# Performance work log

Hardware: AMD Instinct MI355X
Metric: run time of the kernel (lower is better)

## Reference

```python
import jax, jax.numpy as jnp
import numpy as np

B, T, H = 16, 64, 256  # batch, timesteps (= num stacked layers), hidden
L = T                  # MultiRNNCell([cell]*timesteps): layers == timesteps, shared weights


def setup_inputs() -> dict:
    key = jax.random.key(0)
    k1, k2, k3 = jax.random.split(key, 3)
    x = jax.random.normal(k1, (B, T, H), dtype=jnp.float32)
    init_state = jax.random.normal(k2, (L, 2, B, H), dtype=jnp.float32) * 0.1  # [L, (c,h), B, H]
    W = jax.random.normal(k3, (2 * H, 4 * H), dtype=jnp.float32) / np.sqrt(2 * H)
    b = jnp.zeros((4 * H,), dtype=jnp.float32)
    return {"x": x, "init_state": init_state, "W": W, "b": b}


def reference(x, init_state, W, b):
    # TF LSTMCell math: gates order (i, j, f, o), forget_bias = 1.0
    c0 = init_state[:, 0]  # [L,B,H]
    h0 = init_state[:, 1]  # [L,B,H]

    def layer_fn(inp, st):
        # inp: [B,H] input to this layer; st = (c,h) each [B,H]
        lc, lh = st
        z = jnp.concatenate([inp, lh], axis=-1) @ W + b  # [B,4H]
        i, j, f, o = jnp.split(z, 4, axis=-1)
        nc = jax.nn.sigmoid(f + 1.0) * lc + jax.nn.sigmoid(i) * jnp.tanh(j)
        nh = jax.nn.sigmoid(o) * jnp.tanh(nc)
        return nh, (nc, nh)  # carry = input to next layer; ys = new per-layer state

    def step(carry, xt):
        # carry: (c,h) each [L,B,H]; xt: [B,H]
        c, h = carry
        top_h, (nc, nh) = jax.lax.scan(layer_fn, xt, (c, h))
        return (nc, nh), top_h

    (_, _), ys = jax.lax.scan(step, (c0, h0), jnp.transpose(x, (1, 0, 2)))  # ys: [T,B,H]
    return jnp.transpose(ys, (1, 0, 2))  # [B,T,H] top-layer outputs (dynamic_rnn outputs)
```

## Files before the change

### kernel.cpp

```cpp
#include <hip/hip_runtime.h>

typedef _Float16 half8 __attribute__((ext_vector_type(8)));
typedef float f32x4 __attribute__((ext_vector_type(4)));

#define SCOPE __HIP_MEMORY_SCOPE_AGENT

constexpr size_t OFF_FLAGS = 0;
constexpr size_t OFF_H     = 65536;

__device__ __forceinline__ size_t Hidx(int slot, int l, int b, int u) {
  return (((size_t)slot * 64 + l) * 16 + b) * 256 + u;
}
__device__ __forceinline__ float sigm(float v) { return 1.0f / (1.0f + __expf(-v)); }
__device__ __forceinline__ float tanh_(float v) { return 1.0f - 2.0f / (__expf(2.0f * v) + 1.0f); }

__global__ void init_ws(const float* __restrict__ init_state, char* ws) {
  int* flags = (int*)(ws + OFF_FLAGS);
  _Float16* Hp = (_Float16*)(ws + OFF_H);
  const int tid = blockIdx.x * 256 + threadIdx.x;
  if (tid < 4096) flags[tid] = 0;
  for (int e = tid; e < 64 * 16 * 256; e += 65536) {
    const int u = e & 255, b = (e >> 8) & 15, l = e >> 12;
    Hp[Hidx(1, l, b, u)] = (_Float16)init_state[((l * 2 + 1) * 16 + b) * 256 + u];
  }
}

__device__ __forceinline__ void spin_ge4(int* p) {
  for (int it = 0; it < 4000000; ++it) {
    if (__hip_atomic_load(p, __ATOMIC_RELAXED, SCOPE) >= 4) return;
    __builtin_amdgcn_s_sleep(1);
  }
}

__global__ __launch_bounds__(256, 1) void lstm_mfma(
    const float* __restrict__ x, const float* __restrict__ init_state,
    const float* __restrict__ W, const float* __restrict__ bias,
    float* __restrict__ out, char* ws) {
  int* flags = (int*)(ws + OFF_FLAGS);
  unsigned long long* Hp64 = (unsigned long long*)(ws + OFF_H);

  const int tid = threadIdx.x;
  const int wg = blockIdx.x;
  const int l = wg >> 2, r = wg & 3;
  const int wv = tid >> 6, lane = tid & 63;

  __shared__ alignas(16) _Float16 aLds[16 * 64 * 8];
  __shared__ alignas(16) float zLds[16 * 260];
  __shared__ unsigned short hLds[16 * 64];

  half8 wreg[64];
#pragma unroll
  for (int q = 0; q < 4; ++q) {
    const int nl = (wv * 4 + q) * 16 + (lane & 15);
    const int col = (nl & 3) * 256 + r * 64 + (nl >> 2);
#pragma unroll
    for (int kb = 0; kb < 16; ++kb) {
      const int k0 = kb * 32 + (lane >> 4) * 8;
      const float* src = W + (size_t)k0 * 1024 + col;
      half8 hv;
#pragma unroll
      for (int jj = 0; jj < 8; ++jj) hv[jj] = (_Float16)src[(size_t)jj * 1024];
      wreg[q * 16 + kb] = hv;
    }
  }

  const int hu = tid & 63, b4 = tid >> 6;
  const int gu = r * 64 + hu;
  float creg[4];
#pragma unroll
  for (int bi = 0; bi < 4; ++bi)
    creg[bi] = init_state[((l * 2 + 0) * 16 + (b4 * 4 + bi)) * 256 + gu];
  const float bi_ = bias[0 * 256 + gu], bj_ = bias[1 * 256 + gu];
  const float bf_ = bias[2 * 256 + gu], bo_ = bias[3 * 256 + gu];

  for (int t = 0; t < 64; ++t) {
    const int slotCur = t & 1, slotPrev = (t + 1) & 1;

    if (tid == 0) {
      if (l > 0) spin_ge4(&flags[(l - 1) * 64 + t]);
      if (t > 0) spin_ge4(&flags[l * 64 + (t - 1)]);
      if (t >= 2 && l < 63) spin_ge4(&flags[(l + 1) * 64 + (t - 2)]);
    }
    __syncthreads();

#pragma unroll
    for (int i = 0; i < 4; ++i) {
      const int e = i * 256 + tid;
      const int kb = e >> 6, ln = e & 63;
      const int m = ln & 15, k0 = kb * 32 + (ln >> 4) * 8;
      _Float16* dst = &aLds[(size_t)(kb * 64 + ln) * 8];
      if (kb < 8) {
        if (l == 0) {
          const float* xs = x + ((size_t)m * 64 + t) * 256 + k0;
          half8 hv;
#pragma unroll
          for (int jj = 0; jj < 8; ++jj) hv[jj] = (_Float16)xs[jj];
          *(half8*)dst = hv;
        } else {
          const size_t b64 = Hidx(slotCur, l - 1, m, k0) >> 2;
          unsigned long long a0 = __hip_atomic_load(Hp64 + b64, __ATOMIC_RELAXED, SCOPE);
          unsigned long long a1 = __hip_atomic_load(Hp64 + b64 + 1, __ATOMIC_RELAXED, SCOPE);
          ((unsigned long long*)dst)[0] = a0;
          ((unsigned long long*)dst)[1] = a1;
        }
      } else {
        const size_t b64 = Hidx(slotPrev, l, m, k0 - 256) >> 2;
        unsigned long long a0 = __hip_atomic_load(Hp64 + b64, __ATOMIC_RELAXED, SCOPE);
        unsigned long long a1 = __hip_atomic_load(Hp64 + b64 + 1, __ATOMIC_RELAXED, SCOPE);
        ((unsigned long long*)dst)[0] = a0;
        ((unsigned long long*)dst)[1] = a1;
      }
    }
    __syncthreads();

    f32x4 acc[4] = {{0.f, 0.f, 0.f, 0.f}, {0.f, 0.f, 0.f, 0.f},
                    {0.f, 0.f, 0.f, 0.f}, {0.f, 0.f, 0.f, 0.f}};
#pragma unroll
    for (int kb = 0; kb < 16; ++kb) {
      half8 a = *(const half8*)&aLds[(kb * 64 + lane) * 8];
#pragma unroll
      for (int q = 0; q < 4; ++q)
        acc[q] = __builtin_amdgcn_mfma_f32_16x16x32_f16(a, wreg[q * 16 + kb], acc[q], 0, 0, 0);
    }

#pragma unroll
    for (int q = 0; q < 4; ++q) {
      const int nl = (wv * 4 + q) * 16 + (lane & 15);
      const int m0 = (lane >> 4) * 4;
#pragma unroll
      for (int rg = 0; rg < 4; ++rg) zLds[(m0 + rg) * 260 + nl] = acc[q][rg];
    }
    __syncthreads();

#pragma unroll
    for (int bi = 0; bi < 4; ++bi) {
      const int b = b4 * 4 + bi;
      f32x4 zg = *(const f32x4*)&zLds[b * 260 + hu * 4];
      const float iv = zg[0] + bi_, jv = zg[1] + bj_;
      const float fv = zg[2] + bf_, ov = zg[3] + bo_;
      const float nc = sigm(fv + 1.0f) * creg[bi] + sigm(iv) * tanh_(jv);
      const float nh = sigm(ov) * tanh_(nc);
      creg[bi] = nc;
      union { _Float16 f; unsigned short s; } cv;
      cv.f = (_Float16)nh;
      hLds[b * 64 + hu] = cv.s;
      if (l == 63) out[((size_t)b * 64 + t) * 256 + gu] = nh;
    }
    __syncthreads();

    {
      const int b = tid >> 4, u0 = (tid & 15) * 4;
      unsigned long long v = *(unsigned long long*)&hLds[b * 64 + u0];
      __hip_atomic_store(Hp64 + (Hidx(slotCur, l, b, r * 64 + u0) >> 2), v,
                         __ATOMIC_RELAXED, SCOPE);
    }
    __syncthreads();
    if (tid == 0)
      __hip_atomic_fetch_add(&flags[l * 64 + t], 1, __ATOMIC_RELEASE, SCOPE);
  }
}

extern "C" void kernel_launch(void* const* d_in, const int* in_sizes, int n_in,
                              void* d_out, int out_size, void* d_ws,
                              size_t ws_size, hipStream_t stream) {
  const float* x          = (const float*)d_in[0];
  const float* init_state = (const float*)d_in[1];
  const float* W          = (const float*)d_in[2];
  const float* bias       = (const float*)d_in[3];
  float* out = (float*)d_out;
  char* ws   = (char*)d_ws;

  init_ws<<<256, 256, 0, stream>>>(init_state, ws);
  lstm_mfma<<<256, 256, 0, stream>>>(x, init_state, W, bias, out, ws);
}
```

Measured before the change: 784.7 us.

## Replace flag counters with timestep-tagged data words for LSTM wavefront sync

Replaces the per-(layer,timestep) counter flags, spun on by a single thread, with 64-bit words that pack two fp16 hidden values and a 16-bit timestep tag. Each thread polls its own input words until the tags match, so data and readiness arrive in one load. The intent is to drop the release/acquire handoff and the extra barrier and store round-trip on the critical path between layers. It adds a per-workgroup progress counter for backpressure and a slow-path check. It doubles the bytes per hidden value and relies on the 64-bit relaxed atomic stores being seen whole by readers.

```diff
diff --git a/kernel.cpp b/kernel.cpp
--- a/kernel.cpp
+++ b/kernel.cpp
@@ -5,30 +5,29 @@
 
 #define SCOPE __HIP_MEMORY_SCOPE_AGENT
 
-constexpr size_t OFF_FLAGS = 0;
-constexpr size_t OFF_H     = 65536;
-
-__device__ __forceinline__ size_t Hidx(int slot, int l, int b, int u) {
-  return (((size_t)slot * 64 + l) * 16 + b) * 256 + u;
+constexpr size_t OFF_PROG = 0;
+constexpr size_t OFF_H    = 65536;
+constexpr size_t SLOT_STRIDE = (size_t)64 * 16 * 128;
+
+__device__ __forceinline__ size_t Widx(int l, int b, int wi) {
+  return ((size_t)l * 16 + b) * 128 + wi;
 }
 __device__ __forceinline__ float sigm(float v) { return 1.0f / (1.0f + __expf(-v)); }
 __device__ __forceinline__ float tanh_(float v) { return 1.0f - 2.0f / (__expf(2.0f * v) + 1.0f); }
 
 __global__ void init_ws(const float* __restrict__ init_state, char* ws) {
-  int* flags = (int*)(ws + OFF_FLAGS);
-  _Float16* Hp = (_Float16*)(ws + OFF_H);
+  int* prog = (int*)(ws + OFF_PROG);
+  unsigned long long* Hw = (unsigned long long*)(ws + OFF_H);
   const int tid = blockIdx.x * 256 + threadIdx.x;
-  if (tid < 4096) flags[tid] = 0;
-  for (int e = tid; e < 64 * 16 * 256; e += 65536) {
-    const int u = e & 255, b = (e >> 8) & 15, l = e >> 12;
-    Hp[Hidx(1, l, b, u)] = (_Float16)init_state[((l * 2 + 1) * 16 + b) * 256 + u];
-  }
-}
-
-__device__ __forceinline__ void spin_ge4(int* p) {
-  for (int it = 0; it < 4000000; ++it) {
-    if (__hip_atomic_load(p, __ATOMIC_RELAXED, SCOPE) >= 4) return;
-    __builtin_amdgcn_s_sleep(1);
+  if (tid < 256) prog[tid] = -1;
+  for (int e = tid; e < 64 * 16 * 128; e += 65536) {
+    const int wi = e & 127, b = (e >> 7) & 15, l = e >> 11;
+    Hw[Widx(l, b, wi)] = 0xFFFE00000000ULL;
+    union { _Float16 f; unsigned short s; } h0, h1;
+    h0.f = (_Float16)init_state[((l * 2 + 1) * 16 + b) * 256 + 2 * wi];
+    h1.f = (_Float16)init_state[((l * 2 + 1) * 16 + b) * 256 + 2 * wi + 1];
+    Hw[SLOT_STRIDE + Widx(l, b, wi)] =
+        (unsigned long long)h0.s | ((unsigned long long)h1.s << 16) | (0xFFFFULL << 32);
   }
 }
 
@@ -36,8 +35,8 @@
     const float* __restrict__ x, const float* __restrict__ init_state,
     const float* __restrict__ W, const float* __restrict__ bias,
     float* __restrict__ out, char* ws) {
-  int* flags = (int*)(ws + OFF_FLAGS);
-  unsigned long long* Hp64 = (unsigned long long*)(ws + OFF_H);
+  int* prog = (int*)(ws + OFF_PROG);
+  unsigned long long* Hw = (unsigned long long*)(ws + OFF_H);
 
   const int tid = threadIdx.x;
   const int wg = blockIdx.x;
@@ -68,50 +67,96 @@
   const int gu = r * 64 + hu;
   float creg[4];
 #pragma unroll
-  for (int bi = 0; bi < 4; ++bi)
-    creg[bi] = init_state[((l * 2 + 0) * 16 + (b4 * 4 + bi)) * 256 + gu];
+  for (int bb = 0; bb < 4; ++bb)
+    creg[bb] = init_state[((l * 2 + 0) * 16 + (b4 * 4 + bb)) * 256 + gu];
   const float bi_ = bias[0 * 256 + gu], bj_ = bias[1 * 256 + gu];
   const float bf_ = bias[2 * 256 + gu], bo_ = bias[3 * 256 + gu];
 
+  int kbA[4], lnA[4];
+  size_t wbase[4];
+#pragma unroll
+  for (int i = 0; i < 4; ++i) {
+    const int e = i * 256 + tid, kb = e >> 6, ln = e & 63;
+    const int m = ln & 15, k0 = kb * 32 + (ln >> 4) * 8;
+    kbA[i] = kb; lnA[i] = ln;
+    wbase[i] = (i < 2) ? (l > 0 ? Widx(l - 1, m, k0 >> 1) : 0)
+                       : Widx(l, m, (k0 - 256) >> 1);
+  }
+
   for (int t = 0; t < 64; ++t) {
     const int slotCur = t & 1, slotPrev = (t + 1) & 1;
-
-    if (tid == 0) {
-      if (l > 0) spin_ge4(&flags[(l - 1) * 64 + t]);
-      if (t > 0) spin_ge4(&flags[l * 64 + (t - 1)]);
-      if (t >= 2 && l < 63) spin_ge4(&flags[(l + 1) * 64 + (t - 2)]);
+    const unsigned short tagIn = (unsigned short)t;
+    const unsigned short tagOwn = (unsigned short)(t - 1);
+
+    if (l == 0) {
+#pragma unroll
+      for (int i = 0; i < 2; ++i) {
+        const int kb = kbA[i], ln = lnA[i];
+        const int m = ln & 15, k0 = kb * 32 + (ln >> 4) * 8;
+        const float* xs = x + ((size_t)m * 64 + t) * 256 + k0;
+        half8 hv;
+#pragma unroll
+        for (int jj = 0; jj < 8; ++jj) hv[jj] = (_Float16)xs[jj];
+        *(half8*)&aLds[(size_t)(kb * 64 + ln) * 8] = hv;
+      }
+    }
+
+    unsigned pend = (l == 0) ? 0xFF00u : 0xFFFFu;
+    bool bp = !(tid == 0 && l < 63 && t >= 2);
+    int round = 0;
+    while (pend || !bp) {
+      bool fast = true;
+      if (round >= 2 && l > 0 && (pend & 0x00FFu)) {
+        int pl = __hip_atomic_load(&prog[(l - 1) * 4 + r], __ATOMIC_RELAXED, SCOPE);
+        fast = (pl >= t);
+      }
+      if (fast && pend) {
+        unsigned long long wv_[16];
+#pragma unroll
+        for (int i = 0; i < 4; ++i) {
+          const unsigned long long* sp =
+              Hw + ((i < 2 ? slotCur : slotPrev) ? SLOT_STRIDE : 0) + wbase[i];
+#pragma unroll
+          for (int j = 0; j < 4; ++j) {
+            const int b_ = i * 4 + j;
+            if ((pend >> b_) & 1u)
+              wv_[b_] = __hip_atomic_load(sp + j, __ATOMIC_RELAXED, SCOPE);
+          }
+        }
+#pragma unroll
+        for (int i = 0; i < 4; ++i) {
+          unsigned* dp = (unsigned*)&aLds[(size_t)(kbA[i] * 64 + lnA[i]) * 8];
+          const unsigned short exp_ = (i < 2) ? tagIn : tagOwn;
+#pragma unroll
+          for (int j = 0; j < 4; ++j) {
+            const int b_ = i * 4 + j;
+            if ((pend >> b_) & 1u) {
+              const unsigned long long wd = wv_[b_];
+              if ((unsigned short)(wd >> 32) == exp_) {
+                dp[j] = (unsigned)wd;
+                pend &= ~(1u << b_);
+              }
+            }
+          }
+        }
+      }
+      if (!bp) {
+        const int need = t - 2;
+        int p0 = __hip_atomic_load(&prog[(l + 1) * 4 + 0], __ATOMIC_RELAXED, SCOPE);
+        int p1 = __hip_atomic_load(&prog[(l + 1) * 4 + 1], __ATOMIC_RELAXED, SCOPE);
+        int p2 = __hip_atomic_load(&prog[(l + 1) * 4 + 2], __ATOMIC_RELAXED, SCOPE);
+        int p3 = __hip_atomic_load(&prog[(l + 1) * 4 + 3], __ATOMIC_RELAXED, SCOPE);
+        bp = (p0 >= need) && (p1 >= need) && (p2 >= need) && (p3 >= need);
+      }
+      if (pend || !bp) {
+        ++round;
+        if (round > 4000000) break;
+        if (fast) __builtin_amdgcn_s_sleep(1);
+        else      __builtin_amdgcn_s_sleep(16);
+      }
     }
     __syncthreads();
-
-#pragma unroll
-    for (int i = 0; i < 4; ++i) {
-      const int e = i * 256 + tid;
-      const int kb = e >> 6, ln = e & 63;
-      const int m = ln & 15, k0 = kb * 32 + (ln >> 4) * 8;
-      _Float16* dst = &aLds[(size_t)(kb * 64 + ln) * 8];
-      if (kb < 8) {
-        if (l == 0) {
-          const float* xs = x + ((size_t)m * 64 + t) * 256 + k0;
-          half8 hv;
-#pragma unroll
-          for (int jj = 0; jj < 8; ++jj) hv[jj] = (_Float16)xs[jj];
-          *(half8*)dst = hv;
-        } else {
-          const size_t b64 = Hidx(slotCur, l - 1, m, k0) >> 2;
-          unsigned long long a0 = __hip_atomic_load(Hp64 + b64, __ATOMIC_RELAXED, SCOPE);
-          unsigned long long a1 = __hip_atomic_load(Hp64 + b64 + 1, __ATOMIC_RELAXED, SCOPE);
-          ((unsigned long long*)dst)[0] = a0;
-          ((unsigned long long*)dst)[1] = a1;
-        }
-      } else {
-        const size_t b64 = Hidx(slotPrev, l, m, k0 - 256) >> 2;
-        unsigned long long a0 = __hip_atomic_load(Hp64 + b64, __ATOMIC_RELAXED, SCOPE);
-        unsigned long long a1 = __hip_atomic_load(Hp64 + b64 + 1, __ATOMIC_RELAXED, SCOPE);
-        ((unsigned long long*)dst)[0] = a0;
-        ((unsigned long long*)dst)[1] = a1;
-      }
-    }
-    __syncthreads();
+    if (tid == 0) __hip_atomic_store(&prog[wg], t, __ATOMIC_RELAXED, SCOPE);
 
     f32x4 acc[4] = {{0.f, 0.f, 0.f, 0.f}, {0.f, 0.f, 0.f, 0.f},
                     {0.f, 0.f, 0.f, 0.f}, {0.f, 0.f, 0.f, 0.f}};
@@ -133,14 +178,14 @@
     __syncthreads();
 
 #pragma unroll
-    for (int bi = 0; bi < 4; ++bi) {
-      const int b = b4 * 4 + bi;
+    for (int bb = 0; bb < 4; ++bb) {
+      const int b = b4 * 4 + bb;
       f32x4 zg = *(const f32x4*)&zLds[b * 260 + hu * 4];
       const float iv = zg[0] + bi_, jv = zg[1] + bj_;
       const float fv = zg[2] + bf_, ov = zg[3] + bo_;
-      const float nc = sigm(fv + 1.0f) * creg[bi] + sigm(iv) * tanh_(jv);
+      const float nc = sigm(fv + 1.0f) * creg[bb] + sigm(iv) * tanh_(jv);
       const float nh = sigm(ov) * tanh_(nc);
-      creg[bi] = nc;
+      creg[bb] = nc;
       union { _Float16 f; unsigned short s; } cv;
       cv.f = (_Float16)nh;
       hLds[b * 64 + hu] = cv.s;
@@ -149,14 +194,17 @@
     __syncthreads();
 
     {
-      const int b = tid >> 4, u0 = (tid & 15) * 4;
-      unsigned long long v = *(unsigned long long*)&hLds[b * 64 + u0];
-      __hip_atomic_store(Hp64 + (Hidx(slotCur, l, b, r * 64 + u0) >> 2), v,
-                         __ATOMIC_RELAXED, SCOPE);
-    }
-    __syncthreads();
-    if (tid == 0)
-      __hip_atomic_fetch_add(&flags[l * 64 + t], 1, __ATOMIC_RELEASE, SCOPE);
+      const int b = tid >> 4, lw0 = (tid & 15) * 2;
+#pragma unroll
+      for (int q = 0; q < 2; ++q) {
+        const int lw = lw0 + q, u0 = 2 * lw;
+        unsigned lo = (unsigned)hLds[b * 64 + u0] | ((unsigned)hLds[b * 64 + u0 + 1] << 16);
+        unsigned long long wd =
+            (unsigned long long)lo | ((unsigned long long)tagIn << 32);
+        __hip_atomic_store(Hw + (slotCur ? SLOT_STRIDE : 0) + Widx(l, b, r * 32 + lw),
+                           wd, __ATOMIC_RELAXED, SCOPE);
+      }
+    }
   }
 }
 
```

Result: slower. 813.2 us (+3.6%).

## Replace flag counters with epoch-tagged hidden-state words and register-side gate shuffles

Applied to the files above, without the earlier changes.

Each hidden-state element is now stored as a 32-bit word carrying an epoch/timestep tag, so consumers poll the data itself instead of waiting on per-layer flag counters. The readiness wait is spread across all waves, and back-pressure uses a per-workgroup progress array with cached minimums. The gate reshuffle now goes through lane shuffles instead of an LDS round trip, which removes two barriers. The cost is twice the global traffic per hidden element, polling loops with timeouts, and an extra epoch-bump kernel per launch.

```diff
diff --git a/kernel.cpp b/kernel.cpp
--- a/kernel.cpp
+++ b/kernel.cpp
@@ -2,33 +2,46 @@
 
 typedef _Float16 half8 __attribute__((ext_vector_type(8)));
 typedef float f32x4 __attribute__((ext_vector_type(4)));
-
-#define SCOPE __HIP_MEMORY_SCOPE_AGENT
-
-constexpr size_t OFF_FLAGS = 0;
+typedef unsigned int u32;
+typedef unsigned int u32x4 __attribute__((ext_vector_type(4)));
+
+#define SC_AGENT __HIP_MEMORY_SCOPE_AGENT
+
+constexpr size_t OFF_PROG  = 0;
+constexpr size_t OFF_EPOCH = 4096;
 constexpr size_t OFF_H     = 65536;
-
-__device__ __forceinline__ size_t Hidx(int slot, int l, int b, int u) {
-  return (((size_t)slot * 64 + l) * 16 + b) * 256 + u;
-}
+constexpr size_t S4 = (size_t)64 * 16 * 256;
+
 __device__ __forceinline__ float sigm(float v) { return 1.0f / (1.0f + __expf(-v)); }
 __device__ __forceinline__ float tanh_(float v) { return 1.0f - 2.0f / (__expf(2.0f * v) + 1.0f); }
 
+#define GLD4(dst, base, OFS)                                                  \
+  asm volatile("global_load_dwordx4 %0, %1, off offset:" #OFS " sc0 sc1"      \
+               : "=v"(dst) : "v"(base))
+
+__global__ void bump_epoch(char* ws) {
+  u32* ep = (u32*)(ws + OFF_EPOCH);
+  u32 v = __hip_atomic_load(ep, __ATOMIC_RELAXED, SC_AGENT);
+  u32 n = (v + 1) & 0x1FFu;
+  if (n == 0) n = 1;
+  __hip_atomic_store(ep, n, __ATOMIC_RELAXED, SC_AGENT);
+}
+
 __global__ void init_ws(const float* __restrict__ init_state, char* ws) {
-  int* flags = (int*)(ws + OFF_FLAGS);
-  _Float16* Hp = (_Float16*)(ws + OFF_H);
+  u32* prog = (u32*)(ws + OFF_PROG);
+  u32* Hw4 = (u32*)(ws + OFF_H);
+  const u32 ep = __hip_atomic_load((u32*)(ws + OFF_EPOCH), __ATOMIC_RELAXED, SC_AGENT);
+  const u32 epb = (ep & 0x1FFu) << 7;
   const int tid = blockIdx.x * 256 + threadIdx.x;
-  if (tid < 4096) flags[tid] = 0;
+  if (tid < 256) prog[tid] = epb - 1u;
+  const u32 tagInit = (epb | 127u) << 16;
   for (int e = tid; e < 64 * 16 * 256; e += 65536) {
     const int u = e & 255, b = (e >> 8) & 15, l = e >> 12;
-    Hp[Hidx(1, l, b, u)] = (_Float16)init_state[((l * 2 + 1) * 16 + b) * 256 + u];
-  }
-}
-
-__device__ __forceinline__ void spin_ge4(int* p) {
-  for (int it = 0; it < 4000000; ++it) {
-    if (__hip_atomic_load(p, __ATOMIC_RELAXED, SCOPE) >= 4) return;
-    __builtin_amdgcn_s_sleep(1);
+    const size_t idx = ((size_t)l * 16 + b) * 256 + u;
+    Hw4[idx] = 0u;
+    union { _Float16 f; unsigned short s; } hv;
+    hv.f = (_Float16)init_state[((l * 2 + 1) * 16 + b) * 256 + u];
+    Hw4[S4 + idx] = (u32)hv.s | tagInit;
   }
 }
 
@@ -36,17 +49,18 @@
     const float* __restrict__ x, const float* __restrict__ init_state,
     const float* __restrict__ W, const float* __restrict__ bias,
     float* __restrict__ out, char* ws) {
-  int* flags = (int*)(ws + OFF_FLAGS);
-  unsigned long long* Hp64 = (unsigned long long*)(ws + OFF_H);
+  u32* prog = (u32*)(ws + OFF_PROG);
+  u32* Hw4 = (u32*)(ws + OFF_H);
 
   const int tid = threadIdx.x;
   const int wg = blockIdx.x;
   const int l = wg >> 2, r = wg & 3;
   const int wv = tid >> 6, lane = tid & 63;
 
+  const u32 epb = (__hip_atomic_load((u32*)(ws + OFF_EPOCH), __ATOMIC_RELAXED,
+                                     SC_AGENT) & 0x1FFu) << 7;
+
   __shared__ alignas(16) _Float16 aLds[16 * 64 * 8];
-  __shared__ alignas(16) float zLds[16 * 260];
-  __shared__ unsigned short hLds[16 * 64];
 
   half8 wreg[64];
 #pragma unroll
@@ -64,54 +78,120 @@
     }
   }
 
-  const int hu = tid & 63, b4 = tid >> 6;
-  const int gu = r * 64 + hu;
-  float creg[4];
-#pragma unroll
-  for (int bi = 0; bi < 4; ++bi)
-    creg[bi] = init_state[((l * 2 + 0) * 16 + (b4 * 4 + bi)) * 256 + gu];
-  const float bi_ = bias[0 * 256 + gu], bj_ = bias[1 * 256 + gu];
-  const float bf_ = bias[2 * 256 + gu], bo_ = bias[3 * 256 + gu];
+  const int m_own = (lane >> 4) * 4 + (lane & 3);
+  int gu_q[4];
+  float creg[4], bI[4], bJ[4], bF[4], bO[4];
+#pragma unroll
+  for (int q = 0; q < 4; ++q) {
+    const int u_q = (wv * 4 + q) * 4 + ((lane & 15) >> 2);
+    gu_q[q] = r * 64 + u_q;
+    creg[q] = init_state[((l * 2 + 0) * 16 + m_own) * 256 + gu_q[q]];
+    bI[q] = bias[0 * 256 + gu_q[q]];
+    bJ[q] = bias[1 * 256 + gu_q[q]];
+    bF[q] = bias[2 * 256 + gu_q[q]];
+    bO[q] = bias[3 * 256 + gu_q[q]];
+  }
+
+  const int m = lane & 15;
+  const int ksub = (lane >> 4) * 8;
+
+  u32 plCache = 0, bpCache = 0;
 
   for (int t = 0; t < 64; ++t) {
     const int slotCur = t & 1, slotPrev = (t + 1) & 1;
-
-    if (tid == 0) {
-      if (l > 0) spin_ge4(&flags[(l - 1) * 64 + t]);
-      if (t > 0) spin_ge4(&flags[l * 64 + (t - 1)]);
-      if (t >= 2 && l < 63) spin_ge4(&flags[(l + 1) * 64 + (t - 2)]);
+    const u32 expIn = epb | (u32)t;
+    const u32 expOwn = (t > 0) ? (epb | (u32)(t - 1)) : (epb | 127u);
+
+    if (l == 0) {
+#pragma unroll
+      for (int i = 0; i < 2; ++i) {
+        const int kb = i * 4 + wv;
+        const int k0 = kb * 32 + ksub;
+        const float* xs = x + ((size_t)m * 64 + t) * 256 + k0;
+        half8 hv;
+#pragma unroll
+        for (int jj = 0; jj < 8; ++jj) hv[jj] = (_Float16)xs[jj];
+        *(half8*)&aLds[(size_t)(kb * 64 + lane) * 8] = hv;
+      }
+    }
+
+    if (l > 0 && plCache < (epb | (u32)t)) {
+      u32* pb = &prog[(l - 1) * 4];
+      int g = 0;
+      while (true) {
+        u32x4 pv;
+        GLD4(pv, pb, 0);
+        asm volatile("s_waitcnt vmcnt(0)" ::: "memory");
+        __builtin_amdgcn_sched_barrier(0);
+        u32 mn = pv[0] < pv[1] ? pv[0] : pv[1];
+        mn = mn < pv[2] ? mn : pv[2];
+        mn = mn < pv[3] ? mn : pv[3];
+        plCache = mn;
+        if (mn >= (epb | (u32)t)) break;
+        __builtin_amdgcn_s_sleep(4);
+        if (++g > 800000) break;
+      }
+    }
+
+    if (tid == 0 && l < 63 && t >= 2 && bpCache < (epb | (u32)(t - 2))) {
+      u32* pb = &prog[(l + 1) * 4];
+      int g = 0;
+      while (true) {
+        u32x4 pv;
+        GLD4(pv, pb, 0);
+        asm volatile("s_waitcnt vmcnt(0)" ::: "memory");
+        __builtin_amdgcn_sched_barrier(0);
+        u32 mn = pv[0] < pv[1] ? pv[0] : pv[1];
+        mn = mn < pv[2] ? mn : pv[2];
+        mn = mn < pv[3] ? mn : pv[3];
+        bpCache = mn;
+        if (mn >= (epb | (u32)(t - 2))) break;
+        __builtin_amdgcn_s_sleep(2);
+        if (++g > 800000) break;
+      }
+    }
+
+    unsigned pend = (l == 0) ? 0xF0u : 0xFFu;
+    const u32* pLow = Hw4 + (slotCur ? S4 : 0) +
+                      (((size_t)(l > 0 ? l - 1 : 0) * 16 + m) * 256) + wv * 32 + ksub;
+    const u32* pHigh = Hw4 + (slotPrev ? S4 : 0) +
+                       (((size_t)l * 16 + m) * 256) + wv * 32 + ksub;
+    int round = 0;
+    while (pend) {
+      u32x4 gv[8];
+      if (pend & 0x01u) GLD4(gv[0], pLow, 0);
+      if (pend & 0x02u) GLD4(gv[1], pLow, 16);
+      if (pend & 0x04u) GLD4(gv[2], pLow, 512);
+      if (pend & 0x08u) GLD4(gv[3], pLow, 528);
+      if (pend & 0x10u) GLD4(gv[4], pHigh, 0);
+      if (pend & 0x20u) GLD4(gv[5], pHigh, 16);
+      if (pend & 0x40u) GLD4(gv[6], pHigh, 512);
+      if (pend & 0x80u) GLD4(gv[7], pHigh, 528);
+      asm volatile("s_waitcnt vmcnt(0)" ::: "memory");
+      __builtin_amdgcn_sched_barrier(0);
+#pragma unroll
+      for (int b = 0; b < 8; ++b) {
+        if ((pend >> b) & 1u) {
+          const u32 exp_ = (b < 4) ? expIn : expOwn;
+          const u32x4 v = gv[b];
+          if ((v[0] >> 16) == exp_ && (v[1] >> 16) == exp_ &&
+              (v[2] >> 16) == exp_ && (v[3] >> 16) == exp_) {
+            const int kb = (b >> 1) * 4 + wv;
+            u32* dp = (u32*)&aLds[(size_t)(kb * 64 + lane) * 8 + (b & 1) * 4];
+            dp[0] = (v[0] & 0xFFFFu) | (v[1] << 16);
+            dp[1] = (v[2] & 0xFFFFu) | (v[3] << 16);
+            pend &= ~(1u << b);
+          }
+        }
+      }
+      if (pend) {
+        if (++round > 500000) break;
+        if (round > 32 && (round & 3) == 0) __builtin_amdgcn_s_sleep(1);
+      }
     }
     __syncthreads();
-
-#pragma unroll
-    for (int i = 0; i < 4; ++i) {
-      const int e = i * 256 + tid;
-      const int kb = e >> 6, ln = e & 63;
-      const int m = ln & 15, k0 = kb * 32 + (ln >> 4) * 8;
-      _Float16* dst = &aLds[(size_t)(kb * 64 + ln) * 8];
-      if (kb < 8) {
-        if (l == 0) {
-          const float* xs = x + ((size_t)m * 64 + t) * 256 + k0;
-          half8 hv;
-#pragma unroll
-          for (int jj = 0; jj < 8; ++jj) hv[jj] = (_Float16)xs[jj];
-          *(half8*)dst = hv;
-        } else {
-          const size_t b64 = Hidx(slotCur, l - 1, m, k0) >> 2;
-          unsigned long long a0 = __hip_atomic_load(Hp64 + b64, __ATOMIC_RELAXED, SCOPE);
-          unsigned long long a1 = __hip_atomic_load(Hp64 + b64 + 1, __ATOMIC_RELAXED, SCOPE);
-          ((unsigned long long*)dst)[0] = a0;
-          ((unsigned long long*)dst)[1] = a1;
-        }
-      } else {
-        const size_t b64 = Hidx(slotPrev, l, m, k0 - 256) >> 2;
-        unsigned long long a0 = __hip_atomic_load(Hp64 + b64, __ATOMIC_RELAXED, SCOPE);
-        unsigned long long a1 = __hip_atomic_load(Hp64 + b64 + 1, __ATOMIC_RELAXED, SCOPE);
-        ((unsigned long long*)dst)[0] = a0;
-        ((unsigned long long*)dst)[1] = a1;
-      }
-    }
-    __syncthreads();
+    if (tid == 0)
+      __hip_atomic_store(&prog[l * 4 + r], epb | (u32)t, __ATOMIC_RELAXED, SC_AGENT);
 
     f32x4 acc[4] = {{0.f, 0.f, 0.f, 0.f}, {0.f, 0.f, 0.f, 0.f},
                     {0.f, 0.f, 0.f, 0.f}, {0.f, 0.f, 0.f, 0.f}};
@@ -122,41 +202,35 @@
       for (int q = 0; q < 4; ++q)
         acc[q] = __builtin_amdgcn_mfma_f32_16x16x32_f16(a, wreg[q * 16 + kb], acc[q], 0, 0, 0);
     }
+    __syncthreads();
 
 #pragma unroll
     for (int q = 0; q < 4; ++q) {
-      const int nl = (wv * 4 + q) * 16 + (lane & 15);
-      const int m0 = (lane >> 4) * 4;
-#pragma unroll
-      for (int rg = 0; rg < 4; ++rg) zLds[(m0 + rg) * 260 + nl] = acc[q][rg];
-    }
-    __syncthreads();
-
-#pragma unroll
-    for (int bi = 0; bi < 4; ++bi) {
-      const int b = b4 * 4 + bi;
-      f32x4 zg = *(const f32x4*)&zLds[b * 260 + hu * 4];
-      const float iv = zg[0] + bi_, jv = zg[1] + bj_;
-      const float fv = zg[2] + bf_, ov = zg[3] + bo_;
-      const float nc = sigm(fv + 1.0f) * creg[bi] + sigm(iv) * tanh_(jv);
+      float v0 = acc[q][0], v1 = acc[q][1], v2 = acc[q][2], v3 = acc[q][3];
+      float e0 = __shfl_xor(v1, 1, 64), e1 = __shfl_xor(v0, 1, 64);
+      float e2 = __shfl_xor(v3, 1, 64), e3 = __shfl_xor(v2, 1, 64);
+      const bool o1 = (lane & 1);
+      float m0 = o1 ? e0 : v0, m1 = o1 ? v1 : e1;
+      float m2 = o1 ? e2 : v2, m3 = o1 ? v3 : e3;
+      float f0 = __shfl_xor(m2, 2, 64), f1 = __shfl_xor(m3, 2, 64);
+      float f2 = __shfl_xor(m0, 2, 64), f3 = __shfl_xor(m1, 2, 64);
+      const bool o2 = (lane & 2);
+      float gI = o2 ? f0 : m0, gJ = o2 ? f1 : m1;
+      float gF = o2 ? m2 : f2, gO = o2 ? m3 : f3;
+
+      const float iv = gI + bI[q], jv = gJ + bJ[q];
+      const float fv = gF + bF[q], ov = gO + bO[q];
+      const float nc = sigm(fv + 1.0f) * creg[q] + sigm(iv) * tanh_(jv);
       const float nh = sigm(ov) * tanh_(nc);
-      creg[bi] = nc;
+      creg[q] = nc;
       union { _Float16 f; unsigned short s; } cv;
       cv.f = (_Float16)nh;
-      hLds[b * 64 + hu] = cv.s;
-      if (l == 63) out[((size_t)b * 64 + t) * 256 + gu] = nh;
-    }
-    __syncthreads();
-
-    {
-      const int b = tid >> 4, u0 = (tid & 15) * 4;
-      unsigned long long v = *(unsigned long long*)&hLds[b * 64 + u0];
-      __hip_atomic_store(Hp64 + (Hidx(slotCur, l, b, r * 64 + u0) >> 2), v,
-                         __ATOMIC_RELAXED, SCOPE);
-    }
-    __syncthreads();
-    if (tid == 0)
-      __hip_atomic_fetch_add(&flags[l * 64 + t], 1, __ATOMIC_RELEASE, SCOPE);
+      const size_t idx = (slotCur ? S4 : 0) +
+                         ((size_t)l * 16 + m_own) * 256 + gu_q[q];
+      __hip_atomic_store(Hw4 + idx, (u32)cv.s | (expIn << 16),
+                         __ATOMIC_RELAXED, SC_AGENT);
+      if (l == 63) out[((size_t)m_own * 64 + t) * 256 + gu_q[q]] = nh;
+    }
   }
 }
 
@@ -170,6 +244,7 @@
   float* out = (float*)d_out;
   char* ws   = (char*)d_ws;
 
+  bump_epoch<<<1, 1, 0, stream>>>(ws);
   init_ws<<<256, 256, 0, stream>>>(init_state, ws);
   lstm_mfma<<<256, 256, 0, stream>>>(x, init_state, W, bias, out, ws);
 }
```

Result: faster. 677.1 us (-13.7%).
